# Optimization experiments

Hardware: AMD Instinct MI355X
Metric: run time of the kernel (lower is better)

## Reference

```python
import jax, jax.numpy as jnp
import numpy as np

MASS, CHARGE, ALPHA, BETA = 1.0, 0.5, 0.1, 0.05
ETA = jnp.array([1.0, -1.0, -1.0, -1.0], dtype=jnp.float32)  # Minkowski metric diag


def setup_inputs() -> dict:
    key = jax.random.key(0)
    k1, k2, k3 = jax.random.split(key, 3)
    B = 262144
    y = jax.random.normal(k1, (B, 8), dtype=jnp.float32)
    W = jax.random.normal(k2, (4, 4), dtype=jnp.float32) * 0.3
    V = jax.random.normal(k3, (4, 4), dtype=jnp.float32) * 0.3
    return {"y": y, "W": W, "V": V}


def _lagrangian(z):
    # z = (x, u, A) concatenated, shape [12]
    x, u, A = z[0:4], z[4:8], z[8:12]
    kinetic = 0.5 * MASS * jnp.sum(ETA * u * u)
    coupling = CHARGE * jnp.sum(ETA * u * A)
    xu_term = ALPHA * jnp.sum((x * u) ** 2)      # makes J_xu nontrivial
    uA_term = BETA * jnp.sum(u * A) ** 2          # makes J_Au nontrivial
    return kinetic + coupling + xu_term + uA_term


def reference(y, W, V):
    def A_vec(x):  # vector potential A^mu(x), works on [4] or [B,4]
        return jnp.tanh(x @ W.T) + x @ V.T

    x = y[:, 0:4]   # [B,4] positions
    u = y[:, 4:8]   # [B,4] velocities
    A = A_vec(x)    # [B,4]
    z = jnp.concatenate([x, u, A], axis=1)  # [B,12] = (x,u,A)

    gradL = jax.vmap(jax.grad(_lagrangian))(z)      # [B,12]
    H = jax.vmap(jax.hessian(_lagrangian))(z)       # [B,12,12]

    dL_dx = gradL[:, 0:4]
    dL_dA = gradL[:, 8:12]
    J_xu = H[:, 0:4, 4:8]    # d^2L/(dx^mu du^nu)
    J_uu = H[:, 4:8, 4:8]    # d^2L/(du^mu du^nu)
    J_Au = H[:, 8:12, 4:8]   # d^2L/(dA^mu du^nu)

    # dA_dx[a, nu, i] = dA^i/dx^nu (matches tf.stack(..., axis=2) layout)
    jacA = jax.vmap(jax.jacfwd(A_vec))(x)           # [B, i, nu]
    dA_dx = jnp.transpose(jacA, (0, 2, 1))          # [B, nu, i]

    J_uu_inv = jnp.linalg.pinv(J_uu)                # [B,4,4]

    force = (dL_dx
             + jnp.einsum('ajk,ak->aj', dA_dx, dL_dA)
             - jnp.einsum('ai,aij->aj', u,
                          J_xu + jnp.einsum('ajk,akm->ajm', dA_dx, J_Au)))
    acceleration = jnp.einsum('ai,aij->aj', force, J_uu_inv)  # [B,4]
    return acceleration
```

## Files before the change

### kernel.cpp

```cpp
#include <hip/hip_runtime.h>
#include <math.h>


#define SIX_RCOND 2.86102294921875e-5
#define RCOND     4.76837158203125e-6

__device__ __forceinline__ float rcp_nr(float x) {
    float r = __builtin_amdgcn_rcpf(x);
    r = r * (2.0f - x * r);
    return r;
}

__device__ __forceinline__ void fast_tanh4(const double t[4], double th[4])
{
    const double LOG2E = 1.4426950408889634074;
    const double LN2HI = 6.93147180369123816490e-01;
    const double LN2LO = 1.90821492927058770002e-10;
    double e[4], opp[4];
    #pragma unroll
    for (int j = 0; j < 4; ++j) {
        double a  = fabs(t[j]);
        double z  = -2.0 * a;
        double zc = fmax(z, -64.0);
        double nf = rint(zc * LOG2E);
        double r  = fma(-nf, LN2HI, zc);
        r = fma(-nf, LN2LO, r);
        double p = 2.75573192239858906526e-07;
        p = fma(p, r, 2.75573192239858925110e-06);
        p = fma(p, r, 2.48015873015873015873e-05);
        p = fma(p, r, 1.98412698412698412698e-04);
        p = fma(p, r, 1.38888888888888888889e-03);
        p = fma(p, r, 8.33333333333333333333e-03);
        p = fma(p, r, 4.16666666666666666667e-02);
        p = fma(p, r, 1.66666666666666666667e-01);
        p = fma(p, r, 0.5);
        p = fma(p, r, 1.0);
        p = fma(p, r, 1.0);
        int n = (int)nf;
        double twon = __longlong_as_double(((long long)(1023 + n)) << 52);
        double ez = p * twon;
        ez = (z <= -40.0) ? 0.0 : ez;
        e[j]   = ez;
        opp[j] = 1.0 + ez;
    }
    double p01 = opp[0] * opp[1], p23 = opp[2] * opp[3];
    double rp  = 1.0 / (p01 * p23);
    double inv[4] = { opp[1] * p23 * rp, opp[0] * p23 * rp,
                      p01 * opp[3] * rp, p01 * opp[2] * rp };
    #pragma unroll
    for (int j = 0; j < 4; ++j)
        th[j] = copysign((1.0 - e[j]) * inv[j], t[j]);
}

__device__ __forceinline__ void model_terms_f64(
    const double* sW, const double* sV,
    const double x[4], const double u[4],
    double A[4], double f[4], double d[4])
{
    const double eta[4] = {1.0, -1.0, -1.0, -1.0};
    const double CHG = 0.5, ALPHA = 0.1, BETA = 0.05;
    double t[4], s[4];
    #pragma unroll
    for (int j = 0; j < 4; ++j) {
        double tj = 0.0, sj = 0.0;
        #pragma unroll
        for (int k = 0; k < 4; ++k) {
            tj = fma(sW[j*4+k], x[k], tj);
            sj = fma(sV[j*4+k], x[k], sj);
        }
        t[j] = tj; s[j] = sj;
    }
    double th[4];
    fast_tanh4(t, th);
    double G[4][4];
    #pragma unroll
    for (int j = 0; j < 4; ++j) {
        A[j] = th[j] + s[j];
        double dth = 1.0 - th[j] * th[j];
        #pragma unroll
        for (int k = 0; k < 4; ++k) G[j][k] = fma(dth, sW[j*4+k], sV[j*4+k]);
    }
    double S = 0.0;
    #pragma unroll
    for (int k = 0; k < 4; ++k) S += u[k] * A[k];
    double P[4], R[4], Q[4];
    #pragma unroll
    for (int j = 0; j < 4; ++j) {
        double p = 0.0, r = 0.0, q = 0.0;
        #pragma unroll
        for (int k = 0; k < 4; ++k) {
            p += G[k][j] * u[k];
            r += G[j][k] * u[k];
            q += G[k][j] * (CHG * eta[k]) * u[k];
        }
        P[j] = p; R[j] = r; Q[j] = q;
    }
    double T = 0.0;
    #pragma unroll
    for (int j = 0; j < 4; ++j) T += u[j] * R[j];
    #pragma unroll
    for (int j = 0; j < 4; ++j) {
        f[j] = -2.0 * ALPHA * x[j] * u[j] * u[j]
             + Q[j]
             + 2.0 * BETA * S * P[j]
             - (CHG * eta[j] + 2.0 * BETA * S) * R[j]
             - 2.0 * BETA * A[j] * T;
        d[j] = eta[j] + 2.0 * ALPHA * x[j] * x[j];
    }
}

__device__ __forceinline__ void sm_solve_f64(
    const double d[4], const double A[4], const double f[4], double acc[4])
{
    const double C2 = 0.1;
    double b[4], fd[4], den = 1.0, w = 0.0;
    #pragma unroll
    for (int j = 0; j < 4; ++j) {
        double inv = 1.0 / d[j];
        b[j]  = A[j] * inv;
        fd[j] = f[j] * inv;
        den  += C2 * A[j] * b[j];
        w    += b[j] * f[j];
    }
    double scale = C2 * w / den;
    #pragma unroll
    for (int j = 0; j < 4; ++j) acc[j] = fd[j] - b[j] * scale;
}

__device__ __forceinline__ bool criterion_f64(
    const double d[4], const double A[4])
{
    const double C2 = 0.1;
    double mind = 1e300;
    #pragma unroll
    for (int j = 0; j < 4; ++j) {
        double a = fabs(d[j]);
        mind = (a < mind) ? a : mind;
    }
    double p01 = d[0] * d[1], p23 = d[2] * d[3];
    double det = p01 * p23
        + C2 * (A[0]*A[0]*(d[1]*p23) + A[1]*A[1]*(d[0]*p23) +
                A[2]*A[2]*(p01*d[3]) + A[3]*A[3]*(p01*d[2]));
    double sumA2 = 0.0, sumA4 = 0.0, F2 = 0.0;
    #pragma unroll
    for (int j = 0; j < 4; ++j) {
        double Aj2 = A[j] * A[j];
        sumA2 += Aj2; sumA4 += Aj2 * Aj2;
        double Jjj = d[j] + C2 * Aj2;
        F2 += Jjj * Jjj;
    }
    F2 += C2 * C2 * (sumA2 * sumA2 - sumA4);
    double rowmax = 0.0;
    #pragma unroll
    for (int r = 0; r < 4; ++r) {
        double rs = 0.0;
        #pragma unroll
        for (int c = 0; c < 4; ++c) {
            double Jrc = C2 * A[r] * A[c] + ((r == c) ? d[r] : 0.0);
            rs += fabs(Jrc);
        }
        rowmax = (rs > rowmax) ? rs : rowmax;
    }
    double sig_hi2 = rowmax * rowmax;
    sig_hi2 = (F2 < sig_hi2) ? F2 : sig_hi2;
    return (fabs(det) > SIX_RCOND * sig_hi2 * sig_hi2) && (mind > 1e-3);
}

__device__ __forceinline__ void jacobi_pinv_reg(
    const double d[4], const double A[4], const double f[4], double acc[4])
{
    const double C2 = 0.1;
    double M[4][4], Vm[4][4];
    #pragma unroll
    for (int r = 0; r < 4; ++r) {
        #pragma unroll
        for (int c = 0; c < 4; ++c) {
            M[r][c] = C2 * A[r] * A[c];
            Vm[r][c] = (r == c) ? 1.0 : 0.0;
        }
        M[r][r] += d[r];
    }
    for (int sweep = 0; sweep < 8; ++sweep) {
        #pragma unroll
        for (int p = 0; p < 3; ++p) {
            #pragma unroll
            for (int q2 = p + 1; q2 < 4; ++q2) {
                double apq = M[p][q2];
                bool active = fabs(apq) > 1e-280;
                double div = active ? (2.0 * apq) : 1.0;
                double tau = (M[q2][q2] - M[p][p]) / div;
                double tt = ((tau >= 0.0) ? 1.0 : -1.0) /
                            (fabs(tau) + sqrt(1.0 + tau * tau));
                double c = 1.0 / sqrt(1.0 + tt * tt);
                double s = tt * c;
                c = active ? c : 1.0;
                s = active ? s : 0.0;
                #pragma unroll
                for (int k = 0; k < 4; ++k) {
                    double mkp = M[k][p], mkq = M[k][q2];
                    M[k][p]  = c * mkp - s * mkq;
                    M[k][q2] = s * mkp + c * mkq;
                }
                #pragma unroll
                for (int k = 0; k < 4; ++k) {
                    double mpk = M[p][k], mqk = M[q2][k];
                    M[p][k]  = c * mpk - s * mqk;
                    M[q2][k] = s * mpk + c * mqk;
                }
                #pragma unroll
                for (int k = 0; k < 4; ++k) {
                    double vkp = Vm[k][p], vkq = Vm[k][q2];
                    Vm[k][p]  = c * vkp - s * vkq;
                    Vm[k][q2] = s * vkp + c * vkq;
                }
            }
        }
    }
    double lam[4], sigmax = 0.0;
    #pragma unroll
    for (int k = 0; k < 4; ++k) {
        lam[k] = M[k][k];
        double a = fabs(lam[k]);
        sigmax = (a > sigmax) ? a : sigmax;
    }
    double cutoff = RCOND * sigmax;
    #pragma unroll
    for (int j = 0; j < 4; ++j) acc[j] = 0.0;
    #pragma unroll
    for (int e = 0; e < 4; ++e) {
        double coef = 0.0;
        #pragma unroll
        for (int k = 0; k < 4; ++k) coef += Vm[k][e] * f[k];
        coef /= lam[e];
        coef = (fabs(lam[e]) > cutoff) ? coef : 0.0;
        #pragma unroll
        for (int j = 0; j < 4; ++j) acc[j] += coef * Vm[j][e];
    }
}

__global__ __launch_bounds__(256, 2) void fused_kernel(
    const float* __restrict__ y, const float* __restrict__ W,
    const float* __restrict__ V, float* __restrict__ out,
    unsigned int* __restrict__ cnt, int* __restrict__ list,
    unsigned int cap, int B)
{
    __shared__ float  sW[16],  sV[16];
    __shared__ double sWd[16], sVd[16];
    __shared__ int sList[256];
    __shared__ int sCount;

    if (threadIdx.x == 0) sCount = 0;
    if (threadIdx.x < 16) {
        float w = W[threadIdx.x];
        sW[threadIdx.x]  = w;
        sWd[threadIdx.x] = (double)w;
    } else if (threadIdx.x < 32) {
        float v = V[threadIdx.x - 16];
        sV[threadIdx.x - 16]  = v;
        sVd[threadIdx.x - 16] = (double)v;
    }
    __syncthreads();

    int i = blockIdx.x * blockDim.x + threadIdx.x;
    const float4* y4 = (const float4*)y;

    if (i < B) {
        float4 xv = y4[2 * i];
        float4 uv = y4[2 * i + 1];
        float x[4] = {xv.x, xv.y, xv.z, xv.w};
        float u[4] = {uv.x, uv.y, uv.z, uv.w};

        const float eta[4] = {1.0f, -1.0f, -1.0f, -1.0f};
        const float CHG = 0.5f, ALPHA = 0.1f, BETA = 0.05f, C2 = 0.1f;
        const float NEG2LOG2E = -2.8853900817779268f;

        float t[4], sv[4];
        #pragma unroll
        for (int j = 0; j < 4; ++j) {
            float tj = 0.0f, sj = 0.0f;
            #pragma unroll
            for (int k = 0; k < 4; ++k) {
                tj = fmaf(sW[j*4+k], x[k], tj);
                sj = fmaf(sV[j*4+k], x[k], sj);
            }
            t[j] = tj; sv[j] = sj;
        }
        float A[4], dth[4];
        #pragma unroll
        for (int j = 0; j < 4; ++j) {
            float a  = fabsf(t[j]);
            float e  = __builtin_amdgcn_exp2f(a * NEG2LOG2E);
            float th = copysignf((1.0f - e) * rcp_nr(1.0f + e), t[j]);
            A[j]   = th + sv[j];
            dth[j] = 1.0f - th * th;
        }
        float G[4][4];
        #pragma unroll
        for (int j = 0; j < 4; ++j)
            #pragma unroll
            for (int k = 0; k < 4; ++k)
                G[j][k] = fmaf(dth[j], sW[j*4+k], sV[j*4+k]);

        float S = 0.0f;
        #pragma unroll
        for (int k = 0; k < 4; ++k) S = fmaf(u[k], A[k], S);
        float P[4], R[4], Q[4];
        #pragma unroll
        for (int j = 0; j < 4; ++j) {
            float p = 0.0f, r = 0.0f, q = 0.0f;
            #pragma unroll
            for (int k = 0; k < 4; ++k) {
                p = fmaf(G[k][j], u[k], p);
                r = fmaf(G[j][k], u[k], r);
                q = fmaf(G[k][j] * (CHG * eta[k]), u[k], q);
            }
            P[j] = p; R[j] = r; Q[j] = q;
        }
        float T = 0.0f;
        #pragma unroll
        for (int j = 0; j < 4; ++j) T = fmaf(u[j], R[j], T);
        float f[4], d[4];
        #pragma unroll
        for (int j = 0; j < 4; ++j) {
            f[j] = -2.0f * ALPHA * x[j] * u[j] * u[j]
                 + Q[j]
                 + 2.0f * BETA * S * P[j]
                 - (CHG * eta[j] + 2.0f * BETA * S) * R[j]
                 - 2.0f * BETA * A[j] * T;
            d[j] = eta[j] + 2.0f * ALPHA * x[j] * x[j];
        }

        float mind = fminf(fminf(fabsf(d[0]), fabsf(d[1])),
                           fminf(fabsf(d[2]), fabsf(d[3])));
        float p01 = d[0] * d[1], p23 = d[2] * d[3];
        float prod = p01 * p23;
        float det = prod
            + C2 * (A[0]*A[0]*(d[1]*p23) + A[1]*A[1]*(d[0]*p23) +
                    A[2]*A[2]*(p01*d[3]) + A[3]*A[3]*(p01*d[2]));
        float rowmax = 0.0f;
        #pragma unroll
        for (int r = 0; r < 4; ++r) {
            float rs = 0.0f;
            #pragma unroll
            for (int c = 0; c < 4; ++c) {
                float Jrc = C2 * A[r] * A[c] + ((r == c) ? d[r] : 0.0f);
                rs += fabsf(Jrc);
            }
            rowmax = fmaxf(rs, rowmax);
        }
        float sig2 = rowmax * rowmax;
        bool safe = (fabsf(det) > sig2 * sig2 * (1.0f / 1024.0f)) && (mind > 1e-3f);

        if (safe) {
            float invprod = rcp_nr(prod);
            float invd[4] = { d[1] * p23 * invprod, d[0] * p23 * invprod,
                              p01 * d[3] * invprod, p01 * d[2] * invprod };
            float b[4], fd[4], den = 1.0f, w = 0.0f;
            #pragma unroll
            for (int j = 0; j < 4; ++j) {
                b[j]  = A[j] * invd[j];
                fd[j] = f[j] * invd[j];
                den   = fmaf(C2 * A[j], b[j], den);
                w     = fmaf(b[j], f[j], w);
            }
            float scale = (C2 * w) * rcp_nr(den);
            float4 res;
            res.x = fd[0] - b[0] * scale; res.y = fd[1] - b[1] * scale;
            res.z = fd[2] - b[2] * scale; res.w = fd[3] - b[3] * scale;
            ((float4*)out)[i] = res;
        } else {
            int k = atomicAdd(&sCount, 1);
            sList[k] = i;
        }
    }
    __syncthreads();

    int nd = sCount;
    if ((int)threadIdx.x < nd) {
        int ii = sList[threadIdx.x];
        float4 xv = y4[2 * ii];
        float4 uv = y4[2 * ii + 1];
        double x[4] = {xv.x, xv.y, xv.z, xv.w};
        double u[4] = {uv.x, uv.y, uv.z, uv.w};
        double A[4], f[4], d[4];
        model_terms_f64(sWd, sVd, x, u, A, f, d);

        bool safe64 = criterion_f64(d, A);
        bool deferred = false;
        if (!safe64) {
            unsigned int idx = atomicAdd(cnt, 1u);
            if (idx < cap) { list[idx] = ii; deferred = true; }
        }
        if (!deferred) {
            double acc[4];
            sm_solve_f64(d, A, f, acc);
            float4 res;
            res.x = (float)acc[0]; res.y = (float)acc[1];
            res.z = (float)acc[2]; res.w = (float)acc[3];
            ((float4*)out)[ii] = res;
        }
    }
}

__global__ __launch_bounds__(64, 1) void slow_kernel(
    const float* __restrict__ y, const float* __restrict__ W,
    const float* __restrict__ V, float* __restrict__ out,
    const unsigned int* __restrict__ cnt, const int* __restrict__ list,
    unsigned int cap)
{
    __shared__ double sW[16], sV[16];
    if (threadIdx.x < 16)      sW[threadIdx.x]      = (double)W[threadIdx.x];
    else if (threadIdx.x < 32) sV[threadIdx.x - 16] = (double)V[threadIdx.x - 16];
    __syncthreads();

    unsigned int n = *cnt;
    if (n > cap) n = cap;
    int stride = gridDim.x * blockDim.x;
    for (unsigned int j = blockIdx.x * blockDim.x + threadIdx.x; j < n; j += stride) {
        int i = list[j];
        const float4* y4 = (const float4*)y;
        float4 xv = y4[2 * i];
        float4 uv = y4[2 * i + 1];
        double x[4] = {xv.x, xv.y, xv.z, xv.w};
        double u[4] = {uv.x, uv.y, uv.z, uv.w};
        double A[4], f[4], d[4];
        model_terms_f64(sW, sV, x, u, A, f, d);

        double acc[4];
        jacobi_pinv_reg(d, A, f, acc);

        float4 res;
        res.x = (float)acc[0]; res.y = (float)acc[1];
        res.z = (float)acc[2]; res.w = (float)acc[3];
        ((float4*)out)[i] = res;
    }
}

extern "C" void kernel_launch(void* const* d_in, const int* in_sizes, int n_in,
                              void* d_out, int out_size, void* d_ws, size_t ws_size,
                              hipStream_t stream) {
    const float* y = (const float*)d_in[0];
    const float* W = (const float*)d_in[1];
    const float* V = (const float*)d_in[2];
    float* out = (float*)d_out;
    int B = in_sizes[0] / 8;

    unsigned int* cnt = (unsigned int*)d_ws;
    int* list = (int*)((char*)d_ws + 16);
    unsigned int cap = (ws_size > 16) ? (unsigned int)((ws_size - 16) / sizeof(int)) : 0u;
    if (cap > (unsigned int)B) cap = (unsigned int)B;

    hipMemsetAsync(d_ws, 0, 16, stream);

    int block = 256;
    int grid = (B + block - 1) / block;
    fused_kernel<<<grid, block, 0, stream>>>(y, W, V, out, cnt, list, cap, B);
    slow_kernel<<<128, 64, 0, stream>>>(y, W, V, out, cnt, list, cap);
}
```

Before: 85.68 us.

## Pass precomputed model terms to slow kernel and cut Jacobi sweeps

The fused kernel now writes the f64 model terms (A, f, d) for each deferred sample into a workspace record. The slow kernel reads those records instead of reloading y and recomputing the model terms, so it no longer needs W and V. The Jacobi eigen-solve also drops from 8 to 6 sweeps, which reduces work on the slow path but may leave less converged results for ill-conditioned cases. The workspace now holds fewer records, so cap is smaller.

```diff
diff --git a/kernel.cpp b/kernel.cpp
--- a/kernel.cpp
+++ b/kernel.cpp
@@ -180,7 +180,7 @@
         }
         M[r][r] += d[r];
     }
-    for (int sweep = 0; sweep < 8; ++sweep) {
+    for (int sweep = 0; sweep < 6; ++sweep) {
         #pragma unroll
         for (int p = 0; p < 3; ++p) {
             #pragma unroll
@@ -241,8 +241,8 @@
 __global__ __launch_bounds__(256, 2) void fused_kernel(
     const float* __restrict__ y, const float* __restrict__ W,
     const float* __restrict__ V, float* __restrict__ out,
-    unsigned int* __restrict__ cnt, int* __restrict__ list,
-    unsigned int cap, int B)
+    unsigned int* __restrict__ cnt, double* __restrict__ data,
+    int* __restrict__ idxs, unsigned int cap, int B)
 {
     __shared__ float  sW[16],  sV[16];
     __shared__ double sWd[16], sVd[16];
@@ -389,7 +389,17 @@
         bool deferred = false;
         if (!safe64) {
             unsigned int idx = atomicAdd(cnt, 1u);
-            if (idx < cap) { list[idx] = ii; deferred = true; }
+            if (idx < cap) {
+                double* rec = data + (size_t)idx * 12;
+                #pragma unroll
+                for (int j = 0; j < 4; ++j) rec[j]     = A[j];
+                #pragma unroll
+                for (int j = 0; j < 4; ++j) rec[4 + j] = f[j];
+                #pragma unroll
+                for (int j = 0; j < 4; ++j) rec[8 + j] = d[j];
+                idxs[idx] = ii;
+                deferred = true;
+            }
         }
         if (!deferred) {
             double acc[4];
@@ -403,28 +413,23 @@
 }
 
 __global__ __launch_bounds__(64, 1) void slow_kernel(
-    const float* __restrict__ y, const float* __restrict__ W,
-    const float* __restrict__ V, float* __restrict__ out,
-    const unsigned int* __restrict__ cnt, const int* __restrict__ list,
-    unsigned int cap)
-{
-    __shared__ double sW[16], sV[16];
-    if (threadIdx.x < 16)      sW[threadIdx.x]      = (double)W[threadIdx.x];
-    else if (threadIdx.x < 32) sV[threadIdx.x - 16] = (double)V[threadIdx.x - 16];
-    __syncthreads();
-
+    float* __restrict__ out,
+    const unsigned int* __restrict__ cnt, const double* __restrict__ data,
+    const int* __restrict__ idxs, unsigned int cap)
+{
     unsigned int n = *cnt;
     if (n > cap) n = cap;
     int stride = gridDim.x * blockDim.x;
     for (unsigned int j = blockIdx.x * blockDim.x + threadIdx.x; j < n; j += stride) {
-        int i = list[j];
-        const float4* y4 = (const float4*)y;
-        float4 xv = y4[2 * i];
-        float4 uv = y4[2 * i + 1];
-        double x[4] = {xv.x, xv.y, xv.z, xv.w};
-        double u[4] = {uv.x, uv.y, uv.z, uv.w};
+        const double* rec = data + (size_t)j * 12;
         double A[4], f[4], d[4];
-        model_terms_f64(sW, sV, x, u, A, f, d);
+        #pragma unroll
+        for (int k = 0; k < 4; ++k) A[k] = rec[k];
+        #pragma unroll
+        for (int k = 0; k < 4; ++k) f[k] = rec[4 + k];
+        #pragma unroll
+        for (int k = 0; k < 4; ++k) d[k] = rec[8 + k];
+        int i = idxs[j];
 
         double acc[4];
         jacobi_pinv_reg(d, A, f, acc);
@@ -446,14 +451,19 @@
     int B = in_sizes[0] / 8;
 
     unsigned int* cnt = (unsigned int*)d_ws;
-    int* list = (int*)((char*)d_ws + 16);
-    unsigned int cap = (ws_size > 16) ? (unsigned int)((ws_size - 16) / sizeof(int)) : 0u;
+    unsigned int cap = 0;
+    if (ws_size > 16) {
+        size_t avail = ws_size - 16;
+        cap = (unsigned int)(avail / (12 * sizeof(double) + sizeof(int)));
+    }
     if (cap > (unsigned int)B) cap = (unsigned int)B;
+    double* data = (double*)((char*)d_ws + 16);
+    int* idxs = (int*)((char*)d_ws + 16 + (size_t)cap * 12 * sizeof(double));
 
     hipMemsetAsync(d_ws, 0, 16, stream);
 
     int block = 256;
     int grid = (B + block - 1) / block;
-    fused_kernel<<<grid, block, 0, stream>>>(y, W, V, out, cnt, list, cap, B);
-    slow_kernel<<<128, 64, 0, stream>>>(y, W, V, out, cnt, list, cap);
-}
+    fused_kernel<<<grid, block, 0, stream>>>(y, W, V, out, cnt, data, idxs, cap, B);
+    slow_kernel<<<128, 64, 0, stream>>>(out, cnt, data, idxs, cap);
+}
```

Result: faster. 78.95 us (median of 2 runs) (-7.9%).
